# Optimization experiments

Hardware: AMD Instinct MI355X
Metric: run time of the kernel (lower is better)

## Reference

```python
import jax, jax.numpy as jnp
import numpy as np
import math

B, H, W, C = 8, 112, 112, 192
WS, SHIFT, NH = 7, 3, 6
HD = C // NH
N = WS * WS
NW = (H // WS) * (W // WS)
MLP_HID = 4 * C
LOG100 = math.log(100.0)


def _rel_table():
    ch = np.arange(-(WS - 1), WS, dtype=np.float32)
    t = np.stack(np.meshgrid(ch, ch, indexing='ij')).transpose(1, 2, 0).reshape(-1, 2)
    t = t / float(WS - 1) * 8.0
    t = np.sign(t) * np.log2(np.abs(t) + 1.0) / np.log2(8.0)
    return t.astype(np.float32)  # ((2*WS-1)^2, 2)


def _rel_index():
    coords = np.stack(np.meshgrid(np.arange(WS), np.arange(WS), indexing='ij')).reshape(2, -1)
    rel = (coords[:, :, None] - coords[:, None, :]).transpose(1, 2, 0)
    rel = rel + np.array([WS - 1, WS - 1])
    rel = rel * np.array([2 * WS - 1, 1])
    return rel.sum(-1).astype(np.int32)  # (N, N)


def _attn_mask():
    img = np.zeros((H, W), dtype=np.float32)
    cnt = 0
    for hsl in (slice(0, -WS), slice(-WS, -SHIFT), slice(-SHIFT, None)):
        for wsl in (slice(0, -WS), slice(-WS, -SHIFT), slice(-SHIFT, None)):
            img[hsl, wsl] = cnt
            cnt += 1
    mw = img.reshape(H // WS, WS, W // WS, WS).transpose(0, 2, 1, 3).reshape(-1, N)
    diff = mw[:, None, :] - mw[:, :, None]
    return np.where(diff != 0, -100.0, 0.0).astype(np.float32)  # (NW, N, N)

REL_TABLE = jnp.asarray(_rel_table())
REL_INDEX = jnp.asarray(_rel_index())
ATTN_MASK = jnp.asarray(_attn_mask())


def _ln(v, g, b, eps=1e-5):
    m = jnp.mean(v, axis=-1, keepdims=True)
    s = jnp.mean((v - m) ** 2, axis=-1, keepdims=True)
    return (v - m) / jnp.sqrt(s + eps) * g + b


def setup_inputs() -> dict:
    key = jax.random.key(0)
    ks = jax.random.split(key, 12)
    std = 0.02
    inp = {
        'x': jax.random.normal(ks[0], (B, H * W, C), jnp.float32),
        'q_w': jax.random.normal(ks[1], (C, C), jnp.float32) * std,
        'q_b': jnp.zeros((C,), jnp.float32),
        'k_w': jax.random.normal(ks[2], (C, C), jnp.float32) * std,
        'v_w': jax.random.normal(ks[3], (C, C), jnp.float32) * std,
        'v_b': jnp.zeros((C,), jnp.float32),
        'proj_w': jax.random.normal(ks[4], (C, C), jnp.float32) * std,
        'proj_b': jnp.zeros((C,), jnp.float32),
        'logit_scale': jnp.log(10.0 * jnp.ones((NH, 1, 1), jnp.float32)),
        'cpb_w0': jax.random.normal(ks[5], (2, 512), jnp.float32) * std,
        'cpb_b0': jnp.zeros((512,), jnp.float32),
        'cpb_w1': jax.random.normal(ks[6], (512, NH), jnp.float32) * std,
        'ln1_g': jnp.ones((C,), jnp.float32),
        'ln1_b': jnp.zeros((C,), jnp.float32),
        'ln2_g': jnp.ones((C,), jnp.float32),
        'ln2_b': jnp.zeros((C,), jnp.float32),
        'fc1_w': jax.random.normal(ks[7], (C, MLP_HID), jnp.float32) * std,
        'fc1_b': jnp.zeros((MLP_HID,), jnp.float32),
        'fc2_w': jax.random.normal(ks[8], (MLP_HID, C), jnp.float32) * std,
        'fc2_b': jnp.zeros((C,), jnp.float32),
    }
    return inp


def reference(x, q_w, q_b, k_w, v_w, v_b, proj_w, proj_b, logit_scale,
              cpb_w0, cpb_b0, cpb_w1, ln1_g, ln1_b, ln2_g, ln2_b,
              fc1_w, fc1_b, fc2_w, fc2_b):
    shortcut = x  # (B, L, C)
    h = x.reshape(B, H, W, C)
    # cyclic shift
    h = jnp.roll(h, shift=(-SHIFT, -SHIFT), axis=(1, 2))
    # window partition -> (B*NW, N, C)
    h = h.reshape(B, H // WS, WS, W // WS, WS, C).transpose(0, 1, 3, 2, 4, 5)
    h = h.reshape(B * NW, N, C)

    q = (h @ q_w + q_b).reshape(-1, N, NH, HD).transpose(0, 2, 1, 3)
    k = (h @ k_w).reshape(-1, N, NH, HD).transpose(0, 2, 1, 3)
    v = (h @ v_w + v_b).reshape(-1, N, NH, HD).transpose(0, 2, 1, 3)

    # cosine-similarity attention
    q = q / jnp.maximum(jnp.linalg.norm(q, axis=-1, keepdims=True), 1e-6)
    k = k / jnp.maximum(jnp.linalg.norm(k, axis=-1, keepdims=True), 1e-6)
    scale = jnp.exp(jnp.minimum(logit_scale, LOG100))  # (NH,1,1)
    attn = jnp.einsum('bhqd,bhkd->bhqk', q, k) * scale

    # relative position bias via CPB MLP
    rpb = jax.nn.relu(REL_TABLE @ cpb_w0 + cpb_b0) @ cpb_w1  # (169, NH)
    rpb = rpb[REL_INDEX.reshape(-1)].reshape(N, N, NH).transpose(2, 0, 1)
    rpb = 16.0 * jax.nn.sigmoid(rpb)  # (NH, N, N)
    attn = attn + rpb[None]

    # shift mask
    attn = attn.reshape(B, NW, NH, N, N) + ATTN_MASK[None, :, None]
    attn = attn.reshape(B * NW, NH, N, N)
    attn = jax.nn.softmax(attn, axis=-1)

    out = jnp.einsum('bhqk,bhkd->bhqd', attn, v)
    out = out.transpose(0, 2, 1, 3).reshape(B * NW, N, C)
    out = out @ proj_w + proj_b

    # window reverse + reverse shift
    out = out.reshape(B, H // WS, W // WS, WS, WS, C).transpose(0, 1, 3, 2, 4, 5)
    out = out.reshape(B, H, W, C)
    out = jnp.roll(out, shift=(SHIFT, SHIFT), axis=(1, 2)).reshape(B, H * W, C)

    # post-norm residual (Swin-v2)
    h1 = shortcut + _ln(out, ln1_g, ln1_b)
    mlp = jax.nn.gelu(h1 @ fc1_w + fc1_b) @ fc2_w + fc2_b
    return h1 + _ln(mlp, ln2_g, ln2_b)
```

## Files before the change

### kernel.cpp

```cpp
#include <hip/hip_runtime.h>

typedef unsigned short u16;
typedef unsigned int   u32;
typedef __attribute__((ext_vector_type(8))) short bf16x8;
typedef __attribute__((ext_vector_type(4))) float f32x4;

#define B_      8
#define HW_     112
#define C_      192
#define NH_     6
#define HD_     32
#define L_      (HW_*HW_)
#define M_      (B_*L_)
#define MLP_    768
#define QKVN_   576
#define LOG100_ 4.6051702f
#define LOG2E_  1.44269504f

__device__ __forceinline__ float bf2f(u16 u){
  union { float f; u32 i; } v; v.i = ((u32)u) << 16; return v.f;
}
__device__ __forceinline__ u16 f2bf(float f){
  union { float f; u32 i; } v; v.f = f;
  u32 r = (v.i + 0x7fffu + ((v.i >> 16) & 1u)) >> 16;
  return (u16)r;
}
__device__ __forceinline__ u32 cvtpk(float a, float b){
  u32 r;
  asm("v_cvt_pk_bf16_f32 %0, %1, %2" : "=v"(r) : "v"(a), "v"(b));
  return r;
}
__device__ __forceinline__ void u4_to_f8(uint4 u, float* f){
  f[0]=bf2f((u16)(u.x&0xffffu)); f[1]=bf2f((u16)(u.x>>16));
  f[2]=bf2f((u16)(u.y&0xffffu)); f[3]=bf2f((u16)(u.y>>16));
  f[4]=bf2f((u16)(u.z&0xffffu)); f[5]=bf2f((u16)(u.z>>16));
  f[6]=bf2f((u16)(u.w&0xffffu)); f[7]=bf2f((u16)(u.w>>16));
}

__device__ __forceinline__ int rowelem(int b, int wh, int ww, int t){
  int i = t/7, j = t - i*7;
  int oi = wh*7 + i + 3; if (oi >= 112) oi -= 112;
  int oj = ww*7 + j + 3; if (oj >= 112) oj -= 112;
  return b*L_ + oi*112 + oj;
}

__global__ __launch_bounds__(256) void prep_weights(
    const float* __restrict__ qw, const float* __restrict__ qb,
    const float* __restrict__ kw, const float* __restrict__ vw,
    const float* __restrict__ vb, const float* __restrict__ pw,
    const float* __restrict__ pb, const float* __restrict__ f1w,
    const float* __restrict__ f1b, const float* __restrict__ f2w,
    const float* __restrict__ f2b,
    u16* __restrict__ wt_qkv, float* __restrict__ b_qkv,
    u16* __restrict__ wt_p,   float* __restrict__ b_p,
    u16* __restrict__ wt_f1,  float* __restrict__ b_f1,
    u16* __restrict__ wt_f2,  float* __restrict__ b_f2)
{
  const int S1 = 110592, S2 = 147456, S3 = 294912, S4 = 442368, TOT = 444096;
  int i = blockIdx.x*256 + threadIdx.x;
  if (i >= TOT) return;
  if (i < S1) {
    int n = i/192, k = i%192;
    float v = (n<192) ? qw[k*192+n] : ((n<384) ? kw[k*192+(n-192)] : vw[k*192+(n-384)]);
    wt_qkv[i] = f2bf(v);
  } else if (i < S2) {
    int j = i - S1; int n = j/192, k = j%192;
    wt_p[j] = f2bf(pw[k*192+n]);
  } else if (i < S3) {
    int j = i - S2; int n = j/192, k = j%192;
    wt_f1[j] = f2bf(f1w[k*768+n]);
  } else if (i < S4) {
    int j = i - S3; int n = j/768, k = j%768;
    wt_f2[j] = f2bf(f2w[k*192+n]);
  } else {
    int j = i - S4;
    if (j < 576)        b_qkv[j] = (j<192) ? qb[j] : ((j<384) ? 0.f : vb[j-384]);
    else if (j < 768)   b_p[j-576]   = pb[j-576];
    else if (j < 1536)  b_f1[j-768]  = f1b[j-768];
    else                b_f2[j-1536] = f2b[j-1536];
  }
}

__device__ __forceinline__ float reltab(float x){
  float v = x * (8.f/6.f);
  float r = __log2f(fabsf(v) + 1.f) * (1.f/3.f);
  return (v < 0.f) ? -r : r;
}

__global__ __launch_bounds__(64) void rpb_a_kernel(
    const float* __restrict__ w0, const float* __restrict__ b0,
    const float* __restrict__ w1, float* __restrict__ rpb169)
{
  int tt = blockIdx.x, lane = threadIdx.x;
  float t0 = reltab((float)(tt/13 - 6));
  float t1 = reltab((float)(tt%13 - 6));
  float acc[6] = {0.f,0.f,0.f,0.f,0.f,0.f};
  for (int j = lane; j < 512; j += 64){
    float hid = fmaxf(t0*w0[j] + t1*w0[512+j] + b0[j], 0.f);
#pragma unroll
    for (int h=0; h<6; h++) acc[h] += hid * w1[j*6+h];
  }
#pragma unroll
  for (int h=0; h<6; h++){
#pragma unroll
    for (int m=32; m>=1; m>>=1) acc[h] += __shfl_xor(acc[h], m);
  }
  if (lane == 0){
#pragma unroll
    for (int h=0; h<6; h++) rpb169[tt*6+h] = acc[h];
  }
}

__global__ __launch_bounds__(256) void rpb_b_kernel(
    const float* __restrict__ rpb169, float* __restrict__ biasQ)
{
  int i = blockIdx.x*256 + threadIdx.x;
  if (i >= 98304) return;
  int j = i & 63, q = (i >> 6) & 63;
  int rest = i >> 12;
  int hh = rest % 6, type = rest / 6;
  int kt = j >> 4, s = j & 15;
  int key = ((kt>>1)<<5) + ((s>>2)<<3) + ((kt&1)<<2) + (s&3);
  float val;
  if (key >= 49) val = -60000.f;
  else if (q >= 49) val = 0.f;
  else {
    int qi = q/7, qj = q%7, ki = key/7, kj = key%7;
    int idx = (qi - ki + 6)*13 + (qj - kj + 6);
    float x = rpb169[idx*6 + hh];
    float sig = 16.f / (1.f + __expf(-x));
    int th = type >> 1, tw = type & 1;
    int rq = (th ? (qi<4?1:2) : 0)*3 + (tw ? (qj<4?1:2) : 0);
    int rk = (th ? (ki<4?1:2) : 0)*3 + (tw ? (kj<4?1:2) : 0);
    float msk = (rq != rk) ? -100.f : 0.f;
    val = (sig + msk) * LOG2E_;
  }
  biasQ[i] = val;
}

__device__ __forceinline__ float fast_gelu(float v){
  float t = v*v;
  float w = v * fmaf(-0.1029432f, t, -2.30220817f);
  float e = exp2f(w);
  return v * __builtin_amdgcn_rcpf(1.f + e);
}

#define MODE_GELU 0
#define MODE_LN1  1
#define MODE_LN2  2

template<int K, int MODE>
__global__ __launch_bounds__(512,4) void gemm_fused(
    const u16* __restrict__ A, const u16* __restrict__ Wt,
    const float* __restrict__ bias,
    const float* __restrict__ lng, const float* __restrict__ lnb,
    const float* __restrict__ base32, const u16* __restrict__ base16,
    u16* __restrict__ out16, float* __restrict__ out32, int NN)
{
  __shared__ __align__(16) u16 lds[20480];
  const int tid  = threadIdx.x;
  const int wave = tid >> 6, lane = tid & 63;
  const int m0 = blockIdx.x * 128;
  const int n0 = blockIdx.y * 192;
  const int wr = wave >> 1, wc = wave & 1;
  const int lrow = lane >> 2, lslot = lane & 3;
  const int gk = (lslot ^ ((lrow >> 1) & 3)) * 8;

  const u16* gsrc[3]; u32 ldst[3]; const int nst = (wave < 4) ? 3 : 2;
#pragma unroll
  for (int t=0; t<3; t++){
    int c = wave + t*8;
    if (c < 8)       { gsrc[t] = A  + (size_t)(m0 + c*16 + lrow)*K + gk;      ldst[t] = (u32)(c*512); }
    else if (c < 20) { gsrc[t] = Wt + (size_t)(n0 + (c-8)*16 + lrow)*K + gk;  ldst[t] = (u32)(4096 + (c-8)*512); }
    else             { gsrc[t] = A; ldst[t] = 0; }
  }
  const int lr16 = lane & 15;
  const int lg   = lane >> 4;
  const int slot8 = (lg ^ ((lr16 >> 1) & 3)) * 8;
  u32 aoff[2], boff[6];
#pragma unroll
  for (int mt=0; mt<2; mt++) aoff[mt] = (u32)((wr*32 + mt*16 + lr16)*32 + slot8);
#pragma unroll
  for (int nt=0; nt<6; nt++) boff[nt] = (u32)(4096 + (wc*96 + nt*16 + lr16)*32 + slot8);

  f32x4 acc[2][6];
#pragma unroll
  for (int mt=0; mt<2; mt++)
#pragma unroll
    for (int nt=0; nt<6; nt++)
      acc[mt][nt] = (f32x4){0.f,0.f,0.f,0.f};

  const int NT = K/32;
#define STAGE_F(tt, ph) do { \
  _Pragma("unroll") \
  for (int s_=0; s_<3; s_++) if (s_ < nst) \
    __builtin_amdgcn_global_load_lds( \
        (const __attribute__((address_space(1))) void*)(gsrc[s_] + (tt)*32), \
        (__attribute__((address_space(3))) void*)&lds[ldst[s_] + (ph)], 16, 0, 0); \
} while(0)

  STAGE_F(0, 0u);
  STAGE_F(1, 10240u);

  for (int t=0; t<NT; t++){
    const u32 pb = (u32)(t&1)*10240u;
    if (t+1 < NT){
      if (wave < 4) asm volatile("s_waitcnt vmcnt(3)" ::: "memory");
      else          asm volatile("s_waitcnt vmcnt(2)" ::: "memory");
    } else {
      asm volatile("s_waitcnt vmcnt(0)" ::: "memory");
    }
    __builtin_amdgcn_s_barrier();
    bf16x8 af[2], bf[6];
#pragma unroll
    for (int mt=0; mt<2; mt++) af[mt] = *(const bf16x8*)&lds[pb + aoff[mt]];
#pragma unroll
    for (int nt=0; nt<6; nt++) bf[nt] = *(const bf16x8*)&lds[pb + boff[nt]];
#pragma unroll
    for (int mt=0; mt<2; mt++)
#pragma unroll
      for (int nt=0; nt<6; nt++)
        acc[mt][nt] = __builtin_amdgcn_mfma_f32_16x16x32_bf16(af[mt], bf[nt], acc[mt][nt], 0, 0, 0);
    asm volatile("s_waitcnt lgkmcnt(0)" ::: "memory");
    __builtin_amdgcn_sched_barrier(0);
    __builtin_amdgcn_s_barrier();
    if (t+2 < NT) STAGE_F(t+2, pb);
  }
#undef STAGE_F

#pragma unroll
  for (int nt=0; nt<6; nt++){
    float bsv = bias[n0 + wc*96 + nt*16 + lr16];
#pragma unroll
    for (int mt=0; mt<2; mt++)
#pragma unroll
      for (int r2=0; r2<4; r2++) acc[mt][nt][r2] += bsv;
  }

  if (MODE == MODE_GELU){
#pragma unroll
    for (int mt=0; mt<2; mt++){
      int rbase = m0 + wr*32 + mt*16 + lg*4;
#pragma unroll
      for (int nt=0; nt<6; nt++){
        int col = n0 + wc*96 + nt*16 + lr16;
#pragma unroll
        for (int r2=0; r2<4; r2++)
          out16[(size_t)(rbase + r2)*NN + col] = f2bf(fast_gelu(acc[mt][nt][r2]));
      }
    }
  } else {
    float sv[2][4], sq[2][4];
#pragma unroll
    for (int mt=0; mt<2; mt++)
#pragma unroll
      for (int r2=0; r2<4; r2++){
        float s=0.f, q=0.f;
#pragma unroll
        for (int nt=0; nt<6; nt++){ float x = acc[mt][nt][r2]; s += x; q += x*x; }
        sv[mt][r2]=s; sq[mt][r2]=q;
      }
#pragma unroll
    for (int d=1; d<16; d<<=1){
#pragma unroll
      for (int mt=0; mt<2; mt++)
#pragma unroll
        for (int r2=0; r2<4; r2++){
          sv[mt][r2] += __shfl_xor(sv[mt][r2], d);
          sq[mt][r2] += __shfl_xor(sq[mt][r2], d);
        }
    }
    float* red = (float*)lds;
    __syncthreads();
    if (lr16 == 0){
#pragma unroll
      for (int mt=0; mt<2; mt++)
#pragma unroll
        for (int r2=0; r2<4; r2++){
          int row = wr*32 + mt*16 + lg*4 + r2;
          red[row*4 + wc*2]     = sv[mt][r2];
          red[row*4 + wc*2 + 1] = sq[mt][r2];
        }
    }
    __syncthreads();
    float mean[2][4], rstd[2][4];
#pragma unroll
    for (int mt=0; mt<2; mt++)
#pragma unroll
      for (int r2=0; r2<4; r2++){
        int row = wr*32 + mt*16 + lg*4 + r2;
        float s = red[row*4] + red[row*4+2];
        float q = red[row*4+1] + red[row*4+3];
        float m = s*(1.f/192.f);
        float v = fmaxf(q*(1.f/192.f) - m*m, 0.f);
        mean[mt][r2] = m; rstd[mt][r2] = rsqrtf(v + 1e-5f);
      }
    float gg[6], be[6];
#pragma unroll
    for (int nt=0; nt<6; nt++){
      int col = n0 + wc*96 + nt*16 + lr16;
      gg[nt] = lng[col]; be[nt] = lnb[col];
    }
#pragma unroll
    for (int mt=0; mt<2; mt++){
      int rbase = m0 + wr*32 + mt*16 + lg*4;
#pragma unroll
      for (int nt=0; nt<6; nt++){
        int col = n0 + wc*96 + nt*16 + lr16;
#pragma unroll
        for (int r2=0; r2<4; r2++){
          size_t idx = (size_t)(rbase + r2)*192 + col;
          float r = (acc[mt][nt][r2] - mean[mt][r2])*rstd[mt][r2]*gg[nt] + be[nt];
          if (MODE == MODE_LN1){
            r += base32[idx];
            out16[idx] = f2bf(r);
          } else {
            r += bf2f(base16[idx]);
            out32[idx] = r;
          }
        }
      }
    }
  }
}

__global__ __launch_bounds__(512,4) void gemm_qkv_kernel(
    const float* __restrict__ X, const u16* __restrict__ Wt,
    const float* __restrict__ bias, u16* __restrict__ out)
{
  __shared__ __align__(16) u16 lds[20480];
  const int tid  = threadIdx.x;
  const int wave = tid >> 6, lane = tid & 63;
  const int m0 = blockIdx.x * 128;
  const int n0 = blockIdx.y * 192;
  const int wr = wave >> 1, wc = wave & 1;
  const int lrow = lane >> 2, lslot = lane & 3;
  const int gk = (lslot ^ ((lrow >> 1) & 3)) * 8;

  const u16* gsrcB[2]; u32 ldstB[2]; const int nstB = (wave < 4) ? 2 : 1;
#pragma unroll
  for (int t=0; t<2; t++){
    int c = wave + t*8;
    if (c < 12) { gsrcB[t] = Wt + (size_t)(n0 + c*16 + lrow)*192 + gk; ldstB[t] = (u32)(4096 + c*512); }
    else        { gsrcB[t] = Wt; ldstB[t] = 0; }
  }
  const int ar = tid >> 2, as = tid & 3;
  const float* gA = X + (size_t)(m0 + ar)*192 + as*8;
  const u32 dsta = (u32)(ar*32 + (as ^ ((ar >> 1) & 3))*8);

  const int lr16 = lane & 15;
  const int lg   = lane >> 4;
  const int slot8 = (lg ^ ((lr16 >> 1) & 3)) * 8;
  u32 aoff[2], boff[6];
#pragma unroll
  for (int mt=0; mt<2; mt++) aoff[mt] = (u32)((wr*32 + mt*16 + lr16)*32 + slot8);
#pragma unroll
  for (int nt=0; nt<6; nt++) boff[nt] = (u32)(4096 + (wc*96 + nt*16 + lr16)*32 + slot8);

  f32x4 acc[2][6];
#pragma unroll
  for (int mt=0; mt<2; mt++)
#pragma unroll
    for (int nt=0; nt<6; nt++)
      acc[mt][nt] = (f32x4){0.f,0.f,0.f,0.f};

#define STAGE_B(tt, ph) do { \
  _Pragma("unroll") \
  for (int s_=0; s_<2; s_++) if (s_ < nstB) \
    __builtin_amdgcn_global_load_lds( \
        (const __attribute__((address_space(1))) void*)(gsrcB[s_] + (tt)*32), \
        (__attribute__((address_space(3))) void*)&lds[ldstB[s_] + (ph)], 16, 0, 0); \
} while(0)

  float4 a00 = *(const float4*)gA;
  float4 a01 = *(const float4*)(gA + 4);
  STAGE_B(0, 0u);
  float4 ha0 = *(const float4*)(gA + 32);
  float4 ha1 = *(const float4*)(gA + 36);
  STAGE_B(1, 10240u);
  {
    uint4 aw;
    aw.x = cvtpk(a00.x, a00.y); aw.y = cvtpk(a00.z, a00.w);
    aw.z = cvtpk(a01.x, a01.y); aw.w = cvtpk(a01.z, a01.w);
    *(uint4*)(void*)&lds[dsta] = aw;
  }

  for (int t=0; t<6; t++){
    const u32 pb = (u32)(t&1)*10240u;
    const u32 pn = pb ^ 10240u;
    if (t+1 < 6){
      if (wave < 4) asm volatile("s_waitcnt vmcnt(4)" ::: "memory");
      else          asm volatile("s_waitcnt vmcnt(3)" ::: "memory");
    } else {
      asm volatile("s_waitcnt vmcnt(0)" ::: "memory");
    }
    asm volatile("s_waitcnt lgkmcnt(0)" ::: "memory");
    __builtin_amdgcn_s_barrier();
    bf16x8 af[2], bf[6];
#pragma unroll
    for (int mt=0; mt<2; mt++) af[mt] = *(const bf16x8*)&lds[pb + aoff[mt]];
#pragma unroll
    for (int nt=0; nt<6; nt++) bf[nt] = *(const bf16x8*)&lds[pb + boff[nt]];
#pragma unroll
    for (int mt=0; mt<2; mt++)
#pragma unroll
      for (int nt=0; nt<6; nt++)
        acc[mt][nt] = __builtin_amdgcn_mfma_f32_16x16x32_bf16(af[mt], bf[nt], acc[mt][nt], 0, 0, 0);
    asm volatile("s_waitcnt lgkmcnt(0)" ::: "memory");
    __builtin_amdgcn_sched_barrier(0);
    __builtin_amdgcn_s_barrier();
    float4 na0, na1;
    const bool ld = (t+2 < 6);
    if (ld){
      na0 = *(const float4*)(gA + (t+2)*32);
      na1 = *(const float4*)(gA + (t+2)*32 + 4);
      STAGE_B(t+2, pb);
    }
    if (t+1 < 6){
      uint4 aw;
      aw.x = cvtpk(ha0.x, ha0.y); aw.y = cvtpk(ha0.z, ha0.w);
      aw.z = cvtpk(ha1.x, ha1.y); aw.w = cvtpk(ha1.z, ha1.w);
      *(uint4*)(void*)&lds[pn + dsta] = aw;
    }
    if (ld){ ha0 = na0; ha1 = na1; }
  }
#undef STAGE_B

#pragma unroll
  for (int mt=0; mt<2; mt++){
    int rbase = m0 + wr*32 + mt*16 + lg*4;
#pragma unroll
    for (int nt=0; nt<6; nt++){
      int col = n0 + wc*96 + nt*16 + lr16;
      float bsv = bias[col];
#pragma unroll
      for (int r2=0; r2<4; r2++)
        out[(size_t)(rbase + r2)*QKVN_ + col] = f2bf(acc[mt][nt][r2] + bsv);
    }
  }
}

__global__ __launch_bounds__(64) void attn_kernel(
    const u16* __restrict__ qkv, const float* __restrict__ lsc,
    const float* __restrict__ biasQ, u16* __restrict__ attn_out)
{
  __shared__ __align__(16) u16 smem[2048];
  char* smb = (char*)smem;
  const int id = blockIdx.x;
  const int hh = id % 6;
  const int w  = id / 6;
  const int b  = w >> 8;
  const int wh = (w >> 4) & 15, ww = w & 15;
  const int lane = threadIdx.x;
  const int lg = lane >> 4, lr = lane & 15;
  const int type = ((wh==15)?2:0) + ((ww==15)?1:0);
  const float qscale = __expf(fminf(lsc[hh], LOG100_)) * LOG2E_;

  union BU { bf16x8 v; u32 u[4]; };

  const int myrow = rowelem(b, wh, ww, min(lane, 48));

  const u16* vsrc = qkv + (size_t)myrow*QKVN_ + 384 + hh*32;
  uint4 vld[4];
#pragma unroll
  for (int r=0; r<4; r++) vld[r] = *(const uint4*)(vsrc + r*8);

  int rowq[4], krow[4];
#pragma unroll
  for (int qt=0; qt<4; qt++) rowq[qt] = __shfl(myrow, qt*16 + lr);
#pragma unroll
  for (int kt=0; kt<4; kt++){
    int sig = ((kt>>1)<<5) + ((lr>>2)<<3) + ((kt&1)<<2) + (lr&3);
    krow[kt] = __shfl(myrow, sig);
  }

  bf16x8 qf[4], kf[4];
#pragma unroll
  for (int qt=0; qt<4; qt++){
    const u16* base = qkv + (size_t)rowq[qt]*QKVN_ + hh*32 + lg*8;
    uint4 u = *(const uint4*)base;
    float f[8]; u4_to_f8(u, f);
    float ss = 0.f;
#pragma unroll
    for (int d=0; d<8; d++) ss += f[d]*f[d];
    ss += __shfl_xor(ss, 16); ss += __shfl_xor(ss, 32);
    float rn = qscale * __builtin_amdgcn_rcpf(fmaxf(sqrtf(ss), 1e-6f));
    BU bu;
#pragma unroll
    for (int p=0; p<4; p++) bu.u[p] = cvtpk(f[2*p]*rn, f[2*p+1]*rn);
    qf[qt] = bu.v;
  }
#pragma unroll
  for (int kt=0; kt<4; kt++){
    const u16* base = qkv + (size_t)krow[kt]*QKVN_ + 192 + hh*32 + lg*8;
    uint4 u = *(const uint4*)base;
    float f[8]; u4_to_f8(u, f);
    float ss = 0.f;
#pragma unroll
    for (int d=0; d<8; d++) ss += f[d]*f[d];
    ss += __shfl_xor(ss, 16); ss += __shfl_xor(ss, 32);
    float rn = __builtin_amdgcn_rcpf(fmaxf(sqrtf(ss), 1e-6f));
    BU bu;
#pragma unroll
    for (int p=0; p<4; p++) bu.u[p] = cvtpk(f[2*p]*rn, f[2*p+1]*rn);
    kf[kt] = bu.v;
  }

  f32x4 s2[4][4];
#pragma unroll
  for (int kt=0; kt<4; kt++)
#pragma unroll
    for (int qt=0; qt<4; qt++)
      s2[kt][qt] = __builtin_amdgcn_mfma_f32_16x16x32_bf16(kf[kt], qf[qt],
                     (f32x4){0.f,0.f,0.f,0.f}, 0, 0, 0);

#pragma unroll
  for (int r=0; r<4; r++){
    u32 wds[4] = {vld[r].x, vld[r].y, vld[r].z, vld[r].w};
#pragma unroll
    for (int i=0; i<8; i++){
      int d = r*8 + i;
      u16 val = (u16)(wds[i>>1] >> ((i&1)*16));
      int addr = (d*128 + lane*2) ^ ((d&7)<<4);
      *(u16*)(smb + addr) = val;
    }
  }

  const float* bq = biasQ + (size_t)(type*6 + hh)*4096;
#pragma unroll
  for (int qt=0; qt<4; qt++){
    int q = qt*16 + lr;
#pragma unroll
    for (int kt=0; kt<4; kt++){
      f32x4 bv = *(const f32x4*)(bq + q*64 + kt*16 + lg*4);
      s2[kt][qt] += bv;
    }
  }
#pragma unroll
  for (int qt=0; qt<4; qt++){
    float m = s2[0][qt][0];
#pragma unroll
    for (int kt=0; kt<4; kt++)
#pragma unroll
      for (int r2=0; r2<4; r2++) m = fmaxf(m, s2[kt][qt][r2]);
    m = fmaxf(m, __shfl_xor(m, 16));
    m = fmaxf(m, __shfl_xor(m, 32));
    float sum = 0.f;
#pragma unroll
    for (int kt=0; kt<4; kt++)
#pragma unroll
      for (int r2=0; r2<4; r2++){
        float e = exp2f(s2[kt][qt][r2] - m);
        s2[kt][qt][r2] = e; sum += e;
      }
    sum += __shfl_xor(sum, 16);
    sum += __shfl_xor(sum, 32);
    float rs = __builtin_amdgcn_rcpf(sum);
#pragma unroll
    for (int kt=0; kt<4; kt++)
#pragma unroll
      for (int r2=0; r2<4; r2++) s2[kt][qt][r2] *= rs;
  }

  __syncthreads();

  f32x4 o2[2][4];
#pragma unroll
  for (int dt=0; dt<2; dt++)
#pragma unroll
    for (int qt=0; qt<4; qt++)
      o2[dt][qt] = (f32x4){0.f,0.f,0.f,0.f};

#pragma unroll
  for (int kb=0; kb<2; kb++){
    bf16x8 af[2];
#pragma unroll
    for (int dt=0; dt<2; dt++){
      int d = dt*16 + lr;
      int addr = (d*128 + kb*64 + lg*16) ^ ((d&7)<<4);
      af[dt] = *(const bf16x8*)(smb + addr);
    }
#pragma unroll
    for (int qt=0; qt<4; qt++){
      BU bu;
      bu.u[0] = cvtpk(s2[2*kb][qt][0],   s2[2*kb][qt][1]);
      bu.u[1] = cvtpk(s2[2*kb][qt][2],   s2[2*kb][qt][3]);
      bu.u[2] = cvtpk(s2[2*kb+1][qt][0], s2[2*kb+1][qt][1]);
      bu.u[3] = cvtpk(s2[2*kb+1][qt][2], s2[2*kb+1][qt][3]);
#pragma unroll
      for (int dt=0; dt<2; dt++)
        o2[dt][qt] = __builtin_amdgcn_mfma_f32_16x16x32_bf16(af[dt], bu.v, o2[dt][qt], 0, 0, 0);
    }
  }

#pragma unroll
  for (int qt=0; qt<4; qt++){
    int q = qt*16 + lr;
    if (q < 49){
      u16* op = attn_out + (size_t)rowq[qt]*C_ + hh*32;
#pragma unroll
      for (int dt=0; dt<2; dt++){
        uint2 u2;
        u2.x = cvtpk(o2[dt][qt][0], o2[dt][qt][1]);
        u2.y = cvtpk(o2[dt][qt][2], o2[dt][qt][3]);
        *(uint2*)(void*)(op + dt*16 + lg*4) = u2;
      }
    }
  }
}

extern "C" void kernel_launch(void* const* d_in, const int* in_sizes, int n_in,
                              void* d_out, int out_size, void* d_ws, size_t ws_size,
                              hipStream_t stream)
{
  (void)in_sizes; (void)n_in; (void)out_size; (void)ws_size;
  const float* x      = (const float*)d_in[0];
  const float* q_w    = (const float*)d_in[1];
  const float* q_b    = (const float*)d_in[2];
  const float* k_w    = (const float*)d_in[3];
  const float* v_w    = (const float*)d_in[4];
  const float* v_b    = (const float*)d_in[5];
  const float* proj_w = (const float*)d_in[6];
  const float* proj_b = (const float*)d_in[7];
  const float* lsc    = (const float*)d_in[8];
  const float* cpb_w0 = (const float*)d_in[9];
  const float* cpb_b0 = (const float*)d_in[10];
  const float* cpb_w1 = (const float*)d_in[11];
  const float* ln1_g  = (const float*)d_in[12];
  const float* ln1_b  = (const float*)d_in[13];
  const float* ln2_g  = (const float*)d_in[14];
  const float* ln2_b  = (const float*)d_in[15];
  const float* fc1_w  = (const float*)d_in[16];
  const float* fc1_b  = (const float*)d_in[17];
  const float* fc2_w  = (const float*)d_in[18];
  const float* fc2_b  = (const float*)d_in[19];

  char* ws = (char*)d_ws;
  size_t o = 0;
  u16* qkvb = (u16*)(ws + o);
  u16* mid  = qkvb;              o += 154140672;
  u16* attn_o = (u16*)(ws + o);
  u16* h1b    = attn_o;          o += 38535168;
  u16* wt_qkv = (u16*)(ws + o);  o += 221184;
  float* b_qkv= (float*)(ws + o);o += 2304;
  u16* wt_p   = (u16*)(ws + o);  o += 73728;
  float* b_p  = (float*)(ws + o);o += 768;
  u16* wt_f1  = (u16*)(ws + o);  o += 294912;
  float* b_f1 = (float*)(ws + o);o += 3072;
  u16* wt_f2  = (u16*)(ws + o);  o += 294912;
  float* b_f2 = (float*)(ws + o);o += 768;
  float* rpb169 = (float*)(ws + o); o += 4096;
  float* biasQ  = (float*)(ws + o); o += 393216;

  prep_weights<<<1735, 256, 0, stream>>>(q_w, q_b, k_w, v_w, v_b, proj_w, proj_b,
      fc1_w, fc1_b, fc2_w, fc2_b, wt_qkv, b_qkv, wt_p, b_p, wt_f1, b_f1, wt_f2, b_f2);
  rpb_a_kernel<<<169, 64, 0, stream>>>(cpb_w0, cpb_b0, cpb_w1, rpb169);
  rpb_b_kernel<<<384, 256, 0, stream>>>(rpb169, biasQ);

  gemm_qkv_kernel<<<dim3(784,3), 512, 0, stream>>>(x, wt_qkv, b_qkv, qkvb);
  attn_kernel<<<12288, 64, 0, stream>>>(qkvb, lsc, biasQ, attn_o);
  gemm_fused<192, MODE_LN1><<<dim3(784,1), 512, 0, stream>>>(
      attn_o, wt_p, b_p, ln1_g, ln1_b, x, nullptr, h1b, nullptr, 192);
  gemm_fused<192, MODE_GELU><<<dim3(784,4), 512, 0, stream>>>(
      h1b, wt_f1, b_f1, nullptr, nullptr, nullptr, nullptr, mid, nullptr, 768);
  gemm_fused<768, MODE_LN2><<<dim3(784,1), 512, 0, stream>>>(
      mid, wt_f2, b_f2, ln2_g, ln2_b, nullptr, h1b, nullptr, (float*)d_out, 192);
}
```

Before: 333.4 us.

## Fuse MLP fc1-GELU-fc2-LN2 into one kernel and simplify GEMM pipelining

Replaces the separate fc1+GELU and fc2+LN2 GEMM launches with a single fused kernel. Each 64-row tile keeps its h1 rows and the GELU activation chunk in LDS and accumulates fc2 output in registers across four 192-wide hidden chunks. This removes the round trip of the large 768-wide intermediate through global memory. The existing GEMMs also drop the two-deep prefetch with hand-placed vmcnt waits in favour of a simpler single-ahead double buffer with __syncthreads, which may expose more load latency. The fused kernel uses about 74KB of LDS per block, which limits occupancy.

```diff
diff --git a/kernel.cpp b/kernel.cpp
--- a/kernel.cpp
+++ b/kernel.cpp
@@ -200,17 +200,10 @@
 } while(0)
 
   STAGE_F(0, 0u);
-  STAGE_F(1, 10240u);
-
+  __syncthreads();
   for (int t=0; t<NT; t++){
     const u32 pb = (u32)(t&1)*10240u;
-    if (t+1 < NT){
-      if (wave < 4) asm volatile("s_waitcnt vmcnt(3)" ::: "memory");
-      else          asm volatile("s_waitcnt vmcnt(2)" ::: "memory");
-    } else {
-      asm volatile("s_waitcnt vmcnt(0)" ::: "memory");
-    }
-    __builtin_amdgcn_s_barrier();
+    if (t+1 < NT) STAGE_F(t+1, pb ^ 10240u);
     bf16x8 af[2], bf[6];
 #pragma unroll
     for (int mt=0; mt<2; mt++) af[mt] = *(const bf16x8*)&lds[pb + aoff[mt]];
@@ -221,10 +214,7 @@
 #pragma unroll
       for (int nt=0; nt<6; nt++)
         acc[mt][nt] = __builtin_amdgcn_mfma_f32_16x16x32_bf16(af[mt], bf[nt], acc[mt][nt], 0, 0, 0);
-    asm volatile("s_waitcnt lgkmcnt(0)" ::: "memory");
-    __builtin_amdgcn_sched_barrier(0);
-    __builtin_amdgcn_s_barrier();
-    if (t+2 < NT) STAGE_F(t+2, pb);
+    __syncthreads();
   }
 #undef STAGE_F
 
@@ -271,7 +261,6 @@
         }
     }
     float* red = (float*)lds;
-    __syncthreads();
     if (lr16 == 0){
 #pragma unroll
       for (int mt=0; mt<2; mt++)
@@ -372,30 +361,26 @@
         (__attribute__((address_space(3))) void*)&lds[ldstB[s_] + (ph)], 16, 0, 0); \
 } while(0)
 
-  float4 a00 = *(const float4*)gA;
-  float4 a01 = *(const float4*)(gA + 4);
-  STAGE_B(0, 0u);
-  float4 ha0 = *(const float4*)(gA + 32);
-  float4 ha1 = *(const float4*)(gA + 36);
-  STAGE_B(1, 10240u);
   {
+    float4 a0 = *(const float4*)gA;
+    float4 a1 = *(const float4*)(gA + 4);
+    STAGE_B(0, 0u);
     uint4 aw;
-    aw.x = cvtpk(a00.x, a00.y); aw.y = cvtpk(a00.z, a00.w);
-    aw.z = cvtpk(a01.x, a01.y); aw.w = cvtpk(a01.z, a01.w);
+    aw.x = cvtpk(a0.x, a0.y); aw.y = cvtpk(a0.z, a0.w);
+    aw.z = cvtpk(a1.x, a1.y); aw.w = cvtpk(a1.z, a1.w);
     *(uint4*)(void*)&lds[dsta] = aw;
   }
+  __syncthreads();
 
   for (int t=0; t<6; t++){
     const u32 pb = (u32)(t&1)*10240u;
     const u32 pn = pb ^ 10240u;
-    if (t+1 < 6){
-      if (wave < 4) asm volatile("s_waitcnt vmcnt(4)" ::: "memory");
-      else          asm volatile("s_waitcnt vmcnt(3)" ::: "memory");
-    } else {
-      asm volatile("s_waitcnt vmcnt(0)" ::: "memory");
-    }
-    asm volatile("s_waitcnt lgkmcnt(0)" ::: "memory");
-    __builtin_amdgcn_s_barrier();
+    float4 a0, a1;
+    if (t < 5){
+      a0 = *(const float4*)(gA + (t+1)*32);
+      a1 = *(const float4*)(gA + (t+1)*32 + 4);
+      STAGE_B(t+1, pn);
+    }
     bf16x8 af[2], bf[6];
 #pragma unroll
     for (int mt=0; mt<2; mt++) af[mt] = *(const bf16x8*)&lds[pb + aoff[mt]];
@@ -406,23 +391,13 @@
 #pragma unroll
       for (int nt=0; nt<6; nt++)
         acc[mt][nt] = __builtin_amdgcn_mfma_f32_16x16x32_bf16(af[mt], bf[nt], acc[mt][nt], 0, 0, 0);
-    asm volatile("s_waitcnt lgkmcnt(0)" ::: "memory");
-    __builtin_amdgcn_sched_barrier(0);
-    __builtin_amdgcn_s_barrier();
-    float4 na0, na1;
-    const bool ld = (t+2 < 6);
-    if (ld){
-      na0 = *(const float4*)(gA + (t+2)*32);
-      na1 = *(const float4*)(gA + (t+2)*32 + 4);
-      STAGE_B(t+2, pb);
-    }
-    if (t+1 < 6){
+    if (t < 5){
       uint4 aw;
-      aw.x = cvtpk(ha0.x, ha0.y); aw.y = cvtpk(ha0.z, ha0.w);
-      aw.z = cvtpk(ha1.x, ha1.y); aw.w = cvtpk(ha1.z, ha1.w);
+      aw.x = cvtpk(a0.x, a0.y); aw.y = cvtpk(a0.z, a0.w);
+      aw.z = cvtpk(a1.x, a1.y); aw.w = cvtpk(a1.z, a1.w);
       *(uint4*)(void*)&lds[pn + dsta] = aw;
     }
-    if (ld){ ha0 = na0; ha1 = na1; }
+    __syncthreads();
   }
 #undef STAGE_B
 
@@ -604,6 +579,191 @@
         u2.x = cvtpk(o2[dt][qt][0], o2[dt][qt][1]);
         u2.y = cvtpk(o2[dt][qt][2], o2[dt][qt][3]);
         *(uint2*)(void*)(op + dt*16 + lg*4) = u2;
+      }
+    }
+  }
+}
+
+__global__ __launch_bounds__(256,2) void mlp_fused_kernel(
+    const u16* __restrict__ h1,
+    const u16* __restrict__ wf1,
+    const float* __restrict__ bf1,
+    const u16* __restrict__ wf2,
+    const float* __restrict__ bf2,
+    const float* __restrict__ lng, const float* __restrict__ lnb,
+    float* __restrict__ out)
+{
+  __shared__ __align__(16) char smb[75776];
+  const int tid  = threadIdx.x;
+  const int wave = tid >> 6, lane = tid & 63;
+  const int m0 = blockIdx.x * 64;
+  const int wr = wave >> 1, wc = wave & 1;
+  const int lr16 = lane & 15, lg = lane >> 4;
+  const int lrow = lane >> 2, lslot = lane & 3;
+  const int gko = (lslot ^ ((lrow >> 1) & 3)) * 8;
+  const int slot8 = (lg ^ ((lr16 >> 1) & 3)) * 8;
+
+  {
+    const u16* src = h1 + (size_t)m0*192;
+#pragma unroll
+    for (int j=0; j<6; j++){
+      int i = tid + 256*j;
+      int row = i/24, c8 = i%24;
+      uint4 v = *(const uint4*)(src + i*8);
+      *(uint4*)(smb + row*400 + c8*16) = v;
+    }
+  }
+
+#define STG1(c_, k_, ph_) do { \
+  _Pragma("unroll") \
+  for (int s_=0; s_<3; s_++){ \
+    int ch = wave + s_*4; \
+    const u16* sp = wf1 + (size_t)((c_)*192 + ch*16 + lrow)*192 + (k_)*32 + gko; \
+    __builtin_amdgcn_global_load_lds( \
+        (const __attribute__((address_space(1))) void*)sp, \
+        (__attribute__((address_space(3))) void*)(smb + (ph_) + ch*1024), 16, 0, 0); \
+  } } while(0)
+#define STG2(c_, k_, ph_) do { \
+  _Pragma("unroll") \
+  for (int s_=0; s_<3; s_++){ \
+    int ch = wave + s_*4; \
+    const u16* sp = wf2 + (size_t)(ch*16 + lrow)*768 + (c_)*192 + (k_)*32 + gko; \
+    __builtin_amdgcn_global_load_lds( \
+        (const __attribute__((address_space(1))) void*)sp, \
+        (__attribute__((address_space(3))) void*)(smb + (ph_) + ch*1024), 16, 0, 0); \
+  } } while(0)
+
+  f32x4 oacc[2][6];
+#pragma unroll
+  for (int mt=0; mt<2; mt++)
+#pragma unroll
+    for (int nt=0; nt<6; nt++) oacc[mt][nt] = (f32x4){0.f,0.f,0.f,0.f};
+
+  for (int c=0; c<4; c++){
+    f32x4 macc[2][6];
+#pragma unroll
+    for (int mt=0; mt<2; mt++)
+#pragma unroll
+      for (int nt=0; nt<6; nt++) macc[mt][nt] = (f32x4){0.f,0.f,0.f,0.f};
+
+    STG1(c, 0, 51200u);
+    __syncthreads();
+    for (int k=0; k<6; k++){
+      u32 pb = 51200u + (u32)(k&1)*12288u;
+      if (k < 5) STG1(c, k+1, 51200u + (u32)((k+1)&1)*12288u);
+      bf16x8 af[2], bf[6];
+#pragma unroll
+      for (int mt=0; mt<2; mt++)
+        af[mt] = *(const bf16x8*)(smb + ((wr*32 + mt*16 + lr16)*200 + k*32 + lg*8)*2);
+#pragma unroll
+      for (int nt=0; nt<6; nt++)
+        bf[nt] = *(const bf16x8*)(smb + pb + ((wc*96 + nt*16 + lr16)*32 + slot8)*2);
+#pragma unroll
+      for (int mt=0; mt<2; mt++)
+#pragma unroll
+        for (int nt=0; nt<6; nt++)
+          macc[mt][nt] = __builtin_amdgcn_mfma_f32_16x16x32_bf16(af[mt], bf[nt], macc[mt][nt], 0, 0, 0);
+      __syncthreads();
+    }
+#pragma unroll
+    for (int nt=0; nt<6; nt++){
+      int col = wc*96 + nt*16 + lr16;
+      float bsv = bf1[c*192 + col];
+#pragma unroll
+      for (int mt=0; mt<2; mt++){
+        int row = wr*32 + mt*16 + lg*4;
+#pragma unroll
+        for (int r2=0; r2<4; r2++){
+          float g = fast_gelu(macc[mt][nt][r2] + bsv);
+          *(u16*)(smb + 25600 + ((row + r2)*200 + col)*2) = f2bf(g);
+        }
+      }
+    }
+    STG2(c, 0, 51200u);
+    __syncthreads();
+    for (int k=0; k<6; k++){
+      u32 pb = 51200u + (u32)(k&1)*12288u;
+      if (k < 5) STG2(c, k+1, 51200u + (u32)((k+1)&1)*12288u);
+      bf16x8 af[2], bf[6];
+#pragma unroll
+      for (int mt=0; mt<2; mt++)
+        af[mt] = *(const bf16x8*)(smb + 25600 + ((wr*32 + mt*16 + lr16)*200 + k*32 + lg*8)*2);
+#pragma unroll
+      for (int nt=0; nt<6; nt++)
+        bf[nt] = *(const bf16x8*)(smb + pb + ((wc*96 + nt*16 + lr16)*32 + slot8)*2);
+#pragma unroll
+      for (int mt=0; mt<2; mt++)
+#pragma unroll
+        for (int nt=0; nt<6; nt++)
+          oacc[mt][nt] = __builtin_amdgcn_mfma_f32_16x16x32_bf16(af[mt], bf[nt], oacc[mt][nt], 0, 0, 0);
+      __syncthreads();
+    }
+  }
+#undef STG1
+#undef STG2
+
+#pragma unroll
+  for (int nt=0; nt<6; nt++){
+    float bsv = bf2[wc*96 + nt*16 + lr16];
+#pragma unroll
+    for (int mt=0; mt<2; mt++)
+#pragma unroll
+      for (int r2=0; r2<4; r2++) oacc[mt][nt][r2] += bsv;
+  }
+  float sv[2][4], sq[2][4];
+#pragma unroll
+  for (int mt=0; mt<2; mt++)
+#pragma unroll
+    for (int r2=0; r2<4; r2++){
+      float s=0.f, q=0.f;
+#pragma unroll
+      for (int nt=0; nt<6; nt++){ float x = oacc[mt][nt][r2]; s += x; q += x*x; }
+      sv[mt][r2]=s; sq[mt][r2]=q;
+    }
+#pragma unroll
+  for (int d=1; d<16; d<<=1){
+#pragma unroll
+    for (int mt=0; mt<2; mt++)
+#pragma unroll
+      for (int r2=0; r2<4; r2++){
+        sv[mt][r2] += __shfl_xor(sv[mt][r2], d);
+        sq[mt][r2] += __shfl_xor(sq[mt][r2], d);
+      }
+  }
+  float* red = (float*)(smb + 51200);
+  if (lr16 == 0){
+#pragma unroll
+    for (int mt=0; mt<2; mt++)
+#pragma unroll
+      for (int r2=0; r2<4; r2++){
+        int row = wr*32 + mt*16 + lg*4 + r2;
+        red[row*4 + wc*2]     = sv[mt][r2];
+        red[row*4 + wc*2 + 1] = sq[mt][r2];
+      }
+  }
+  __syncthreads();
+  float gg[6], be[6];
+#pragma unroll
+  for (int nt=0; nt<6; nt++){
+    int col = wc*96 + nt*16 + lr16;
+    gg[nt] = lng[col]; be[nt] = lnb[col];
+  }
+#pragma unroll
+  for (int mt=0; mt<2; mt++){
+#pragma unroll
+    for (int r2=0; r2<4; r2++){
+      int row = wr*32 + mt*16 + lg*4 + r2;
+      float s = red[row*4] + red[row*4+2];
+      float q = red[row*4+1] + red[row*4+3];
+      float mean = s*(1.f/192.f);
+      float var  = fmaxf(q*(1.f/192.f) - mean*mean, 0.f);
+      float rstd = rsqrtf(var + 1e-5f);
+#pragma unroll
+      for (int nt=0; nt<6; nt++){
+        int col = wc*96 + nt*16 + lr16;
+        float base = bf2f(*(const u16*)(smb + (row*200 + col)*2));
+        float r = base + (oacc[mt][nt][r2] - mean)*rstd*gg[nt] + be[nt];
+        out[(size_t)(m0 + row)*192 + col] = r;
       }
     }
   }
@@ -637,8 +797,7 @@
 
   char* ws = (char*)d_ws;
   size_t o = 0;
-  u16* qkvb = (u16*)(ws + o);
-  u16* mid  = qkvb;              o += 154140672;
+  u16* qkvb = (u16*)(ws + o);    o += 154140672;
   u16* attn_o = (u16*)(ws + o);
   u16* h1b    = attn_o;          o += 38535168;
   u16* wt_qkv = (u16*)(ws + o);  o += 221184;
@@ -661,8 +820,6 @@
   attn_kernel<<<12288, 64, 0, stream>>>(qkvb, lsc, biasQ, attn_o);
   gemm_fused<192, MODE_LN1><<<dim3(784,1), 512, 0, stream>>>(
       attn_o, wt_p, b_p, ln1_g, ln1_b, x, nullptr, h1b, nullptr, 192);
-  gemm_fused<192, MODE_GELU><<<dim3(784,4), 512, 0, stream>>>(
-      h1b, wt_f1, b_f1, nullptr, nullptr, nullptr, nullptr, mid, nullptr, 768);
-  gemm_fused<768, MODE_LN2><<<dim3(784,1), 512, 0, stream>>>(
-      mid, wt_f2, b_f2, ln2_g, ln2_b, nullptr, h1b, nullptr, (float*)d_out, 192);
-}
+  mlp_fused_kernel<<<1568, 256, 0, stream>>>(
+      h1b, wt_f1, b_f1, wt_f2, b_f2, ln2_g, ln2_b, (float*)d_out);
+}
```

After: 328.1 us. About the same (-1.6%).
